# Kernel optimization log

Measured on AMD Instinct MI355X. Metric: run time of the kernel, lower is better.

The kernel has to match this reference:

```python
import jax, jax.numpy as jnp
import numpy as np

B, C_IN, H, W = 1024, 3, 32, 32
D_IN = C_IN * H * W          # 3072, matches input_size
R_HID = 128                  # router hidden_size
E = 8                        # num experts
TOP_K = 2
E_HID = 2048                 # expert MLP hidden
N_CLS = 10                   # cifar classes


def setup_inputs() -> dict:
    key = jax.random.key(0)
    ks = jax.random.split(key, 10)
    s = lambda fan_in: 1.0 / np.sqrt(fan_in)
    x = jax.random.normal(ks[0], (B, C_IN, H, W), jnp.float32)
    # router params
    rW1 = jax.random.normal(ks[1], (D_IN, R_HID), jnp.float32) * s(D_IN)
    rb1 = jnp.zeros((R_HID,), jnp.float32)
    rW2 = jax.random.normal(ks[2], (R_HID, E), jnp.float32) * s(R_HID)
    rb2 = jnp.zeros((E,), jnp.float32)
    # stacked expert params [E, ...]
    eW1 = jax.random.normal(ks[3], (E, D_IN, E_HID), jnp.float32) * s(D_IN)
    eb1 = jnp.zeros((E, E_HID), jnp.float32)
    eW2 = jax.random.normal(ks[4], (E, E_HID, N_CLS), jnp.float32) * s(E_HID)
    eb2 = jnp.zeros((E, N_CLS), jnp.float32)
    return {"x": x, "rW1": rW1, "rb1": rb1, "rW2": rW2, "rb2": rb2,
            "eW1": eW1, "eb1": eb1, "eW2": eW2, "eb2": eb2}


def reference(x, rW1, rb1, rW2, rb2, eW1, eb1, eW2, eb2):
    b = x.shape[0]
    xf = x.reshape(b, -1)                                  # [B, D_IN]
    # router (eval mode: no noise, no dropout)
    rh = jax.nn.relu(xf @ rW1 + rb1)
    logits = rh @ rW2 + rb2                                # [B, E]
    rw = jax.nn.softmax(logits, axis=-1)
    w, idx = jax.lax.top_k(rw, TOP_K)                      # [B, K]
    w = w / jnp.sum(w, axis=-1, keepdims=True)
    # dense per-expert compute (same math as masked dispatch)
    eh = jax.nn.relu(jnp.einsum('bd,edh->ebh', xf, eW1) + eb1[:, None, :])  # [E,B,H]
    outs = jnp.einsum('ebh,ehc->ebc', eh, eW2) + eb2[:, None, :]            # [E,B,C]
    # combine: gather each sample's top-k expert outputs
    taken = outs[idx.T, jnp.arange(b)[None, :]]            # [K, B, C]
    return jnp.sum(w.T[:, :, None] * taken, axis=0)        # [B, C]
```

## Files before the change

### kernel.cpp

```cpp
#include <hip/hip_runtime.h>
#include <cstdint>
#include <cstddef>

#define B_TOK 1024
#define DD_IN 3072
#define RHID 128
#define NEXP 8
#define EHID 2048
#define NCLS 10

typedef __attribute__((ext_vector_type(8))) short short8;
typedef __attribute__((ext_vector_type(4))) float floatx4;

__device__ __forceinline__ unsigned short f2bf(float f) {
  unsigned u = __builtin_bit_cast(unsigned, f);
  u += 0x7fffu + ((u >> 16) & 1u);
  return (unsigned short)(u >> 16);
}
__device__ __forceinline__ unsigned pk_bf16(float a, float b) {
  return (unsigned)f2bf(a) | ((unsigned)f2bf(b) << 16);
}
__device__ __forceinline__ float bf2f(unsigned short h) {
  unsigned u = ((unsigned)h) << 16;
  return __builtin_bit_cast(float, u);
}

__global__ __launch_bounds__(256) void k_router_gemm(const float* __restrict__ x,
                                                     const float* __restrict__ rW1,
                                                     float* __restrict__ partial) {
  const int ttile = blockIdx.x;
  const int s = blockIdx.y;
  const int T0 = ttile * 64;
  const int K0 = s * 192;
  __shared__ float xs[16][64];
  __shared__ float wsm[16][132];
  float acc[4][8];
#pragma unroll
  for (int i = 0; i < 4; i++)
#pragma unroll
    for (int j = 0; j < 8; j++) acc[i][j] = 0.f;
  const int tx = threadIdx.x & 15, ty = threadIdx.x >> 4;
  const int tid = threadIdx.x;

  const int xtok = tid >> 2, xk = (tid & 3) << 2;
  const int wk0 = tid >> 5, wf0 = (tid & 31) << 2;

  float4 pX, pW0, pW1;
  pX  = *(const float4*)(x + (size_t)(T0 + xtok) * DD_IN + K0 + xk);
  pW0 = *(const float4*)(rW1 + (size_t)(K0 + wk0) * RHID + wf0);
  pW1 = *(const float4*)(rW1 + (size_t)(K0 + wk0 + 8) * RHID + wf0);

  for (int kc = K0; kc < K0 + 192; kc += 16) {
    xs[xk + 0][xtok] = pX.x; xs[xk + 1][xtok] = pX.y;
    xs[xk + 2][xtok] = pX.z; xs[xk + 3][xtok] = pX.w;
    *(float4*)&wsm[wk0][wf0] = pW0;
    *(float4*)&wsm[wk0 + 8][wf0] = pW1;
    __syncthreads();
    if (kc + 16 < K0 + 192) {
      pX  = *(const float4*)(x + (size_t)(T0 + xtok) * DD_IN + kc + 16 + xk);
      pW0 = *(const float4*)(rW1 + (size_t)(kc + 16 + wk0) * RHID + wf0);
      pW1 = *(const float4*)(rW1 + (size_t)(kc + 16 + wk0 + 8) * RHID + wf0);
    }
#pragma unroll
    for (int kk = 0; kk < 16; kk++) {
      float wv[8], xv[4];
      *(float4*)&wv[0] = *(const float4*)&wsm[kk][tx * 8];
      *(float4*)&wv[4] = *(const float4*)&wsm[kk][tx * 8 + 4];
#pragma unroll
      for (int i = 0; i < 4; i++) xv[i] = xs[kk][ty * 4 + i];
#pragma unroll
      for (int i = 0; i < 4; i++)
#pragma unroll
        for (int j = 0; j < 8; j++) acc[i][j] += xv[i] * wv[j];
    }
    __syncthreads();
  }
#pragma unroll
  for (int i = 0; i < 4; i++) {
    float* p = partial + ((size_t)s * B_TOK + T0 + ty * 4 + i) * RHID + tx * 8;
    *(float4*)p = *(float4*)&acc[i][0];
    *(float4*)(p + 4) = *(float4*)&acc[i][4];
  }
}

__global__ __launch_bounds__(256) void k_router_fin(const float* __restrict__ partial,
                                                    const float* __restrict__ rb1,
                                                    const float* __restrict__ rW2,
                                                    const float* __restrict__ rb2,
                                                    const float* __restrict__ eb2,
                                                    float* __restrict__ out,
                                                    int* __restrict__ cnt,
                                                    int* __restrict__ tokL,
                                                    float* __restrict__ wtL) {
  if (threadIdx.x < 4 * NCLS)
    out[blockIdx.x * 4 * NCLS + threadIdx.x] = eb2[threadIdx.x % NCLS];
  const int lane = threadIdx.x & 63;
  const int tok = blockIdx.x * 4 + (threadIdx.x >> 6);
  float r0 = 0.f, r1 = 0.f;
#pragma unroll
  for (int s = 0; s < 16; s++) {
    const float* p = partial + ((size_t)s * B_TOK + tok) * RHID;
    r0 += p[lane]; r1 += p[lane + 64];
  }
  r0 = fmaxf(r0 + rb1[lane], 0.f);
  r1 = fmaxf(r1 + rb1[lane + 64], 0.f);
  float lg[8];
#pragma unroll
  for (int c = 0; c < 8; c++)
    lg[c] = r0 * rW2[lane * 8 + c] + r1 * rW2[(lane + 64) * 8 + c];
#pragma unroll
  for (int off = 32; off >= 1; off >>= 1)
#pragma unroll
    for (int c = 0; c < 8; c++) lg[c] += __shfl_down(lg[c], off);
  if (lane == 0) {
    float m1 = -1e30f, m2 = -1e30f; int i1 = 0, i2 = 0;
#pragma unroll
    for (int c = 0; c < 8; c++) {
      float l = lg[c] + rb2[c];
      if (l > m1) { m2 = m1; i2 = i1; m1 = l; i1 = c; }
      else if (l > m2) { m2 = l; i2 = c; }
    }
    float w1 = 1.f / (1.f + expf(m2 - m1));
    float w2 = 1.f - w1;
    int p1 = atomicAdd(&cnt[i1], 1);
    tokL[i1 * B_TOK + p1] = tok; wtL[i1 * B_TOK + p1] = w1;
    int p2 = atomicAdd(&cnt[i2], 1);
    tokL[i2 * B_TOK + p2] = tok; wtL[i2 * B_TOK + p2] = w2;
  }
}

__global__ __launch_bounds__(256, 2) void k_expert(const float* __restrict__ x,
                                                   const float* __restrict__ eW1,
                                                   const float* __restrict__ eb1,
                                                   const float* __restrict__ eW2,
                                                   const int* __restrict__ cnt,
                                                   const int* __restrict__ tokL,
                                                   const float* __restrict__ wtL,
                                                   float* __restrict__ out) {
  const int nt = blockIdx.x;
  int mt = blockIdx.y;
  int e = 0;
#pragma unroll
  for (e = 0; e < NEXP; e++) {
    int te = (cnt[e] + 127) >> 7;
    if (mt < te) break;
    mt -= te;
  }
  if (e >= NEXP) return;
  const int cnt_e = cnt[e];

  __shared__ union {
    struct { unsigned short As[128][72]; unsigned Bs[32][132]; } a;
    struct { unsigned short ehs[128][132]; float w2[128 * NCLS]; } b;
  } u;
  __shared__ int stok[128];
  __shared__ float swt[128];

  const int tid = threadIdx.x;
  if (tid < 128) {
    int r = mt * 128 + tid;
    bool v = r < cnt_e;
    stok[tid] = v ? tokL[e * B_TOK + r] : -1;
    swt[tid]  = v ? wtL[e * B_TOK + r] : 0.f;
  }
  __syncthreads();

  const int lane = tid & 63;
  const int wv = tid >> 6;
  const int wm = (wv & 1) * 64, wn = (wv >> 1) * 64;
  const int col = lane & 15, quad = lane >> 4;

  floatx4 acc[4][4];
#pragma unroll
  for (int mi = 0; mi < 4; mi++)
#pragma unroll
    for (int ni = 0; ni < 4; ni++) acc[mi][ni] = (floatx4)0.f;

  const float* W1e = eW1 + (size_t)e * DD_IN * EHID + (size_t)nt * 128;

  const int arow = tid >> 4, ac4 = (tid & 15) << 2;
  const int bk2 = tid >> 5, bn4 = (tid & 31) << 2;

  float4 pA[8];
  float4 pBa[4], pBb[4];

#pragma unroll
  for (int i = 0; i < 8; i++) {
    int tk = stok[arow + i * 16];
    pA[i] = (tk >= 0) ? *(const float4*)(x + (size_t)tk * DD_IN + ac4)
                      : make_float4(0.f, 0.f, 0.f, 0.f);
  }
#pragma unroll
  for (int i = 0; i < 4; i++) {
    const float* src = W1e + (size_t)((bk2 + i * 8) * 2) * EHID + bn4;
    pBa[i] = *(const float4*)src;
    pBb[i] = *(const float4*)(src + EHID);
  }

  for (int k0 = 0; k0 < DD_IN; k0 += 64) {
#pragma unroll
    for (int i = 0; i < 8; i++) {
      uint2 w;
      w.x = pk_bf16(pA[i].x, pA[i].y);
      w.y = pk_bf16(pA[i].z, pA[i].w);
      *(uint2*)&u.a.As[arow + i * 16][ac4] = w;
    }
#pragma unroll
    for (int i = 0; i < 4; i++) {
      uint4 w;
      w.x = pk_bf16(pBa[i].x, pBb[i].x); w.y = pk_bf16(pBa[i].y, pBb[i].y);
      w.z = pk_bf16(pBa[i].z, pBb[i].z); w.w = pk_bf16(pBa[i].w, pBb[i].w);
      *(uint4*)&u.a.Bs[bk2 + i * 8][bn4] = w;
    }
    __syncthreads();
    if (k0 + 64 < DD_IN) {
#pragma unroll
      for (int i = 0; i < 8; i++) {
        int tk = stok[arow + i * 16];
        pA[i] = (tk >= 0) ? *(const float4*)(x + (size_t)tk * DD_IN + k0 + 64 + ac4)
                          : make_float4(0.f, 0.f, 0.f, 0.f);
      }
#pragma unroll
      for (int i = 0; i < 4; i++) {
        const float* src = W1e + (size_t)(k0 + 64 + (bk2 + i * 8) * 2) * EHID + bn4;
        pBa[i] = *(const float4*)src;
        pBb[i] = *(const float4*)(src + EHID);
      }
    }
#pragma unroll
    for (int kk = 0; kk < 2; kk++) {
      short8 af[4], bf[4];
#pragma unroll
      for (int mi = 0; mi < 4; mi++)
        af[mi] = *(const short8*)&u.a.As[wm + mi * 16 + col][kk * 32 + quad * 8];
#pragma unroll
      for (int ni = 0; ni < 4; ni++) {
        int kb = kk * 16 + quad * 4;
        int nb = wn + ni * 16 + col;
        uint4 t;
        t.x = u.a.Bs[kb + 0][nb]; t.y = u.a.Bs[kb + 1][nb];
        t.z = u.a.Bs[kb + 2][nb]; t.w = u.a.Bs[kb + 3][nb];
        bf[ni] = __builtin_bit_cast(short8, t);
      }
#pragma unroll
      for (int mi = 0; mi < 4; mi++)
#pragma unroll
        for (int ni = 0; ni < 4; ni++)
          acc[mi][ni] = __builtin_amdgcn_mfma_f32_16x16x32_bf16(af[mi], bf[ni], acc[mi][ni], 0, 0, 0);
    }
    __syncthreads();
  }
#pragma unroll
  for (int ni = 0; ni < 4; ni++) {
    int hid = wn + ni * 16 + col;
    float bias = eb1[(size_t)e * EHID + nt * 128 + hid];
#pragma unroll
    for (int mi = 0; mi < 4; mi++)
#pragma unroll
      for (int r = 0; r < 4; r++) {
        float val = fmaxf(acc[mi][ni][r] + bias, 0.f);
        u.b.ehs[wm + mi * 16 + quad * 4 + r][hid] = f2bf(val);
      }
  }
#pragma unroll
  for (int i = 0; i < 5; i++) {
    int idx = tid + i * 256;
    if (idx < 128 * NCLS)
      u.b.w2[idx] = eW2[((size_t)e * EHID + nt * 128 + idx / NCLS) * NCLS + (idx % NCLS)];
  }
  __syncthreads();
  {
    int tok = tid >> 1, half = tid & 1;
    float a10[NCLS];
#pragma unroll
    for (int c = 0; c < NCLS; c++) a10[c] = 0.f;
    for (int hh = 0; hh < 64; hh++) {
      int h = half * 64 + hh;
      float eh = bf2f(u.b.ehs[tok][h]);
#pragma unroll
      for (int c = 0; c < NCLS; c++) a10[c] += eh * u.b.w2[h * NCLS + c];
    }
    int tk = stok[tok];
    if (tk >= 0) {
      float wt = swt[tok];
#pragma unroll
      for (int c = 0; c < NCLS; c++)
        atomicAdd(out + (size_t)tk * NCLS + c, wt * a10[c]);
    }
  }
}

extern "C" void kernel_launch(void* const* d_in, const int* in_sizes, int n_in,
                              void* d_out, int out_size, void* d_ws, size_t ws_size,
                              hipStream_t stream) {
  const float* x   = (const float*)d_in[0];
  const float* rW1 = (const float*)d_in[1];
  const float* rb1 = (const float*)d_in[2];
  const float* rW2 = (const float*)d_in[3];
  const float* rb2 = (const float*)d_in[4];
  const float* eW1 = (const float*)d_in[5];
  const float* eb1 = (const float*)d_in[6];
  const float* eW2 = (const float*)d_in[7];
  const float* eb2 = (const float*)d_in[8];
  float* out = (float*)d_out;

  char* ws = (char*)d_ws;
  int*   cnt     = (int*)(ws + 0);
  int*   tokL    = (int*)(ws + 1024);
  float* wtL     = (float*)(ws + 33792);
  float* partial = (float*)(ws + 66560);

  hipMemsetAsync(cnt, 0, 1024, stream);
  k_router_gemm<<<dim3(16, 16), 256, 0, stream>>>(x, rW1, partial);
  k_router_fin<<<256, 256, 0, stream>>>(partial, rb1, rW2, rb2, eb2, out, cnt, tokL, wtL);
  k_expert<<<dim3(16, 23), 256, 0, stream>>>(x, eW1, eb1, eW2, cnt, tokL, wtL, out);
}
```

Baseline: 436.8 us.

## Split expert GEMM over K halves, pre-convert x to bf16, add finalize kernel

The router GEMM now also writes a bf16 copy of x and zeroes the expert counters, which removes the memset and the fp32-to-bf16 conversion inside the expert kernel. The expert GEMM is split-K into two halves over a z grid dimension, which doubles the block count for better occupancy of the CUs. Each half writes bf16 partial hidden activations to workspace. A new finalize kernel sums the halves, applies bias and ReLU, does the second layer and combines results atomically. In exchange there is extra global traffic for the partial activations, an additional launch, and rounding of the pre-activation partials to bf16.

```diff
diff --git a/kernel.cpp b/kernel.cpp
--- a/kernel.cpp
+++ b/kernel.cpp
@@ -8,6 +8,9 @@
 #define NEXP 8
 #define EHID 2048
 #define NCLS 10
+#define KHALF 1536
+#define NTILE_MAX 23
+#define PH_ROWS (NTILE_MAX * 128)
 
 typedef __attribute__((ext_vector_type(8))) short short8;
 typedef __attribute__((ext_vector_type(4))) float floatx4;
@@ -24,10 +27,15 @@
   unsigned u = ((unsigned)h) << 16;
   return __builtin_bit_cast(float, u);
 }
+__device__ __forceinline__ float bflo(unsigned w) { return bf2f((unsigned short)(w & 0xffffu)); }
+__device__ __forceinline__ float bfhi(unsigned w) { return bf2f((unsigned short)(w >> 16)); }
 
 __global__ __launch_bounds__(256) void k_router_gemm(const float* __restrict__ x,
                                                      const float* __restrict__ rW1,
-                                                     float* __restrict__ partial) {
+                                                     float* __restrict__ partial,
+                                                     unsigned short* __restrict__ xbf,
+                                                     int* __restrict__ cnt) {
+  if (blockIdx.x == 0 && blockIdx.y == 0 && threadIdx.x < NEXP) cnt[threadIdx.x] = 0;
   const int ttile = blockIdx.x;
   const int s = blockIdx.y;
   const int T0 = ttile * 64;
@@ -53,6 +61,11 @@
   for (int kc = K0; kc < K0 + 192; kc += 16) {
     xs[xk + 0][xtok] = pX.x; xs[xk + 1][xtok] = pX.y;
     xs[xk + 2][xtok] = pX.z; xs[xk + 3][xtok] = pX.w;
+    {
+      uint2 u2;
+      u2.x = pk_bf16(pX.x, pX.y); u2.y = pk_bf16(pX.z, pX.w);
+      *(uint2*)(xbf + (size_t)(T0 + xtok) * DD_IN + kc + xk) = u2;
+    }
     *(float4*)&wsm[wk0][wf0] = pW0;
     *(float4*)&wsm[wk0 + 8][wf0] = pW1;
     __syncthreads();
@@ -129,39 +142,34 @@
   }
 }
 
-__global__ __launch_bounds__(256, 2) void k_expert(const float* __restrict__ x,
+__global__ __launch_bounds__(256, 2) void k_expert(const unsigned short* __restrict__ xbf,
                                                    const float* __restrict__ eW1,
-                                                   const float* __restrict__ eb1,
-                                                   const float* __restrict__ eW2,
                                                    const int* __restrict__ cnt,
                                                    const int* __restrict__ tokL,
-                                                   const float* __restrict__ wtL,
-                                                   float* __restrict__ out) {
+                                                   unsigned short* __restrict__ ph) {
   const int nt = blockIdx.x;
+  const int z = blockIdx.z;
   int mt = blockIdx.y;
-  int e = 0;
-#pragma unroll
+  int e, base_t = 0;
   for (e = 0; e < NEXP; e++) {
     int te = (cnt[e] + 127) >> 7;
     if (mt < te) break;
-    mt -= te;
+    mt -= te; base_t += te;
   }
   if (e >= NEXP) return;
   const int cnt_e = cnt[e];
+  const int g = base_t + mt;
 
   __shared__ union {
     struct { unsigned short As[128][72]; unsigned Bs[32][132]; } a;
-    struct { unsigned short ehs[128][132]; float w2[128 * NCLS]; } b;
+    unsigned short ehs[128][136];
   } u;
   __shared__ int stok[128];
-  __shared__ float swt[128];
 
   const int tid = threadIdx.x;
   if (tid < 128) {
     int r = mt * 128 + tid;
-    bool v = r < cnt_e;
-    stok[tid] = v ? tokL[e * B_TOK + r] : -1;
-    swt[tid]  = v ? wtL[e * B_TOK + r] : 0.f;
+    stok[tid] = (r < cnt_e) ? tokL[e * B_TOK + r] : 0;
   }
   __syncthreads();
 
@@ -177,34 +185,28 @@
     for (int ni = 0; ni < 4; ni++) acc[mi][ni] = (floatx4)0.f;
 
   const float* W1e = eW1 + (size_t)e * DD_IN * EHID + (size_t)nt * 128;
-
-  const int arow = tid >> 4, ac4 = (tid & 15) << 2;
+  const size_t zb = (size_t)z * KHALF;
+
+  const int arow = tid >> 3, aseg = tid & 7;
   const int bk2 = tid >> 5, bn4 = (tid & 31) << 2;
 
-  float4 pA[8];
+  uint4 pA[4];
   float4 pBa[4], pBb[4];
 
 #pragma unroll
-  for (int i = 0; i < 8; i++) {
-    int tk = stok[arow + i * 16];
-    pA[i] = (tk >= 0) ? *(const float4*)(x + (size_t)tk * DD_IN + ac4)
-                      : make_float4(0.f, 0.f, 0.f, 0.f);
-  }
+  for (int i = 0; i < 4; i++)
+    pA[i] = *(const uint4*)(xbf + (size_t)stok[arow + i * 32] * DD_IN + zb + aseg * 8);
 #pragma unroll
   for (int i = 0; i < 4; i++) {
-    const float* src = W1e + (size_t)((bk2 + i * 8) * 2) * EHID + bn4;
+    const float* src = W1e + (zb + (size_t)((bk2 + i * 8) * 2)) * EHID + bn4;
     pBa[i] = *(const float4*)src;
     pBb[i] = *(const float4*)(src + EHID);
   }
 
-  for (int k0 = 0; k0 < DD_IN; k0 += 64) {
-#pragma unroll
-    for (int i = 0; i < 8; i++) {
-      uint2 w;
-      w.x = pk_bf16(pA[i].x, pA[i].y);
-      w.y = pk_bf16(pA[i].z, pA[i].w);
-      *(uint2*)&u.a.As[arow + i * 16][ac4] = w;
-    }
+  for (int k0 = 0; k0 < KHALF; k0 += 64) {
+#pragma unroll
+    for (int i = 0; i < 4; i++)
+      *(uint4*)&u.a.As[arow + i * 32][aseg * 8] = pA[i];
 #pragma unroll
     for (int i = 0; i < 4; i++) {
       uint4 w;
@@ -213,16 +215,13 @@
       *(uint4*)&u.a.Bs[bk2 + i * 8][bn4] = w;
     }
     __syncthreads();
-    if (k0 + 64 < DD_IN) {
-#pragma unroll
-      for (int i = 0; i < 8; i++) {
-        int tk = stok[arow + i * 16];
-        pA[i] = (tk >= 0) ? *(const float4*)(x + (size_t)tk * DD_IN + k0 + 64 + ac4)
-                          : make_float4(0.f, 0.f, 0.f, 0.f);
-      }
+    if (k0 + 64 < KHALF) {
+#pragma unroll
+      for (int i = 0; i < 4; i++)
+        pA[i] = *(const uint4*)(xbf + (size_t)stok[arow + i * 32] * DD_IN + zb + k0 + 64 + aseg * 8);
 #pragma unroll
       for (int i = 0; i < 4; i++) {
-        const float* src = W1e + (size_t)(k0 + 64 + (bk2 + i * 8) * 2) * EHID + bn4;
+        const float* src = W1e + (zb + (size_t)(k0 + 64 + (bk2 + i * 8) * 2)) * EHID + bn4;
         pBa[i] = *(const float4*)src;
         pBb[i] = *(const float4*)(src + EHID);
       }
@@ -251,42 +250,85 @@
     __syncthreads();
   }
 #pragma unroll
-  for (int ni = 0; ni < 4; ni++) {
-    int hid = wn + ni * 16 + col;
-    float bias = eb1[(size_t)e * EHID + nt * 128 + hid];
+  for (int ni = 0; ni < 4; ni++)
 #pragma unroll
     for (int mi = 0; mi < 4; mi++)
 #pragma unroll
-      for (int r = 0; r < 4; r++) {
-        float val = fmaxf(acc[mi][ni][r] + bias, 0.f);
-        u.b.ehs[wm + mi * 16 + quad * 4 + r][hid] = f2bf(val);
+      for (int r = 0; r < 4; r++)
+        u.ehs[wm + mi * 16 + quad * 4 + r][wn + ni * 16 + col] = f2bf(acc[mi][ni][r]);
+  __syncthreads();
+  unsigned short* dst = ph + ((size_t)z * PH_ROWS + (size_t)g * 128) * EHID + (size_t)nt * 128;
+#pragma unroll
+  for (int i = 0; i < 8; i++) {
+    int s2 = tid + i * 256;
+    int row = s2 >> 4, seg = s2 & 15;
+    *(uint4*)(dst + (size_t)row * EHID + seg * 8) = *(const uint4*)&u.ehs[row][seg * 8];
+  }
+}
+
+__global__ __launch_bounds__(256) void k_finalize(const unsigned short* __restrict__ ph,
+                                                  const float* __restrict__ eb1,
+                                                  const float* __restrict__ eW2,
+                                                  const int* __restrict__ cnt,
+                                                  const int* __restrict__ tokL,
+                                                  const float* __restrict__ wtL,
+                                                  float* __restrict__ out) {
+  const int t = blockIdx.x, hc = blockIdx.y;
+  int mt = t, e;
+  for (e = 0; e < NEXP; e++) {
+    int te = (cnt[e] + 127) >> 7;
+    if (mt < te) break;
+    mt -= te;
+  }
+  if (e >= NEXP) return;
+  const int cnt_e = cnt[e];
+  const int h0 = hc * 256;
+  __shared__ float w2s[256 * NCLS];
+  __shared__ float eb1s[256];
+  const int tid = threadIdx.x;
+#pragma unroll
+  for (int i = 0; i < 10; i++) {
+    int idx = tid + i * 256;
+    w2s[idx] = eW2[((size_t)e * EHID + h0 + idx / NCLS) * NCLS + (idx % NCLS)];
+  }
+  eb1s[tid] = eb1[(size_t)e * EHID + h0 + tid];
+  __syncthreads();
+
+  const int slot = tid >> 1, half = tid & 1;
+  const int r = mt * 128 + slot;
+  const bool valid = r < cnt_e;
+  float a10[NCLS];
+#pragma unroll
+  for (int c = 0; c < NCLS; c++) a10[c] = 0.f;
+
+  const unsigned short* p0 = ph + ((size_t)t * 128 + slot) * EHID + h0 + half * 128;
+  const unsigned short* p1 = p0 + (size_t)PH_ROWS * EHID;
+  if (valid) {
+    for (int hh = 0; hh < 128; hh += 8) {
+      uint4 v0 = *(const uint4*)(p0 + hh);
+      uint4 v1 = *(const uint4*)(p1 + hh);
+      float eh[8];
+      eh[0] = bflo(v0.x) + bflo(v1.x); eh[1] = bfhi(v0.x) + bfhi(v1.x);
+      eh[2] = bflo(v0.y) + bflo(v1.y); eh[3] = bfhi(v0.y) + bfhi(v1.y);
+      eh[4] = bflo(v0.z) + bflo(v1.z); eh[5] = bfhi(v0.z) + bfhi(v1.z);
+      eh[6] = bflo(v0.w) + bflo(v1.w); eh[7] = bfhi(v0.w) + bfhi(v1.w);
+#pragma unroll
+      for (int j = 0; j < 8; j++) {
+        int h = half * 128 + hh + j;
+        float ev = fmaxf(eh[j] + eb1s[h], 0.f);
+#pragma unroll
+        for (int c = 0; c < NCLS; c++) a10[c] += ev * w2s[h * NCLS + c];
       }
-  }
-#pragma unroll
-  for (int i = 0; i < 5; i++) {
-    int idx = tid + i * 256;
-    if (idx < 128 * NCLS)
-      u.b.w2[idx] = eW2[((size_t)e * EHID + nt * 128 + idx / NCLS) * NCLS + (idx % NCLS)];
-  }
-  __syncthreads();
-  {
-    int tok = tid >> 1, half = tid & 1;
-    float a10[NCLS];
-#pragma unroll
-    for (int c = 0; c < NCLS; c++) a10[c] = 0.f;
-    for (int hh = 0; hh < 64; hh++) {
-      int h = half * 64 + hh;
-      float eh = bf2f(u.b.ehs[tok][h]);
-#pragma unroll
-      for (int c = 0; c < NCLS; c++) a10[c] += eh * u.b.w2[h * NCLS + c];
-    }
-    int tk = stok[tok];
-    if (tk >= 0) {
-      float wt = swt[tok];
-#pragma unroll
-      for (int c = 0; c < NCLS; c++)
-        atomicAdd(out + (size_t)tk * NCLS + c, wt * a10[c]);
-    }
+    }
+  }
+#pragma unroll
+  for (int c = 0; c < NCLS; c++) a10[c] += __shfl_down(a10[c], 1);
+  if (valid && half == 0) {
+    int tk = tokL[e * B_TOK + r];
+    float wt = wtL[e * B_TOK + r];
+#pragma unroll
+    for (int c = 0; c < NCLS; c++)
+      atomicAdd(out + (size_t)tk * NCLS + c, wt * a10[c]);
   }
 }
 
@@ -305,13 +347,15 @@
   float* out = (float*)d_out;
 
   char* ws = (char*)d_ws;
-  int*   cnt     = (int*)(ws + 0);
-  int*   tokL    = (int*)(ws + 1024);
-  float* wtL     = (float*)(ws + 33792);
-  float* partial = (float*)(ws + 66560);
-
-  hipMemsetAsync(cnt, 0, 1024, stream);
-  k_router_gemm<<<dim3(16, 16), 256, 0, stream>>>(x, rW1, partial);
+  int*            cnt     = (int*)(ws + 0);
+  int*            tokL    = (int*)(ws + 1024);
+  float*          wtL     = (float*)(ws + 33792);
+  unsigned short* xbf     = (unsigned short*)(ws + 66560);
+  float*          partial = (float*)(ws + 6358016);
+  unsigned short* ph      = (unsigned short*)(ws + 14746624);
+
+  k_router_gemm<<<dim3(16, 16), 256, 0, stream>>>(x, rW1, partial, xbf, cnt);
   k_router_fin<<<256, 256, 0, stream>>>(partial, rb1, rW2, rb2, eb2, out, cnt, tokL, wtL);
-  k_expert<<<dim3(16, 23), 256, 0, stream>>>(x, eW1, eb1, eW2, cnt, tokL, wtL, out);
-}
+  k_expert<<<dim3(16, NTILE_MAX, 2), 256, 0, stream>>>(xbf, eW1, cnt, tokL, ph);
+  k_finalize<<<dim3(NTILE_MAX, 8), 256, 0, stream>>>(ph, eb1, eW2, cnt, tokL, wtL, out);
+}
```

Result: slower. 456.5 us (+4.5%).
